# Performance work log

Measured on AMD Instinct MI355X. Metric: run time of the kernel, lower is better.

Reference implementation:

```python
import jax, jax.numpy as jnp
import numpy as np

B, N, D, H, L = 128, 256, 256, 8, 4      # graphs, nodes/graph, hidden, heads, layers
NTOT = B * N                              # 32768 nodes
E = 1048576                               # edges (avg degree 32)
DIN = 64
DH = D // H
BN_EPS = 1e-5
BN_SCALE = 1.0 / np.sqrt(1.0 + BN_EPS)    # eval BN with running mean 0, var 1


def _bn(h, g, b):
    # eval-mode BatchNorm1d: (h - 0)/sqrt(1 + eps) * g + b
    return h * (g * BN_SCALE) + b


def setup_inputs() -> dict:
    key = jax.random.key(0)
    ks = jax.random.split(key, 32)
    s = 0.02
    x = jax.random.normal(ks[0], (NTOT, DIN), jnp.float32)
    # within-graph random edges: dst lives in the same graph as src
    src = jax.random.randint(ks[1], (E,), 0, NTOT, dtype=jnp.int32)
    dst = (src // N) * N + jax.random.randint(ks[2], (E,), 0, N, dtype=jnp.int32)
    edge_index = jnp.stack([src, dst])
    edge_attr = jax.random.uniform(ks[3], (E,), jnp.float32)
    batch = jnp.arange(NTOT, dtype=jnp.int32) // N
    inp = {
        "x": x,
        "edge_attr": edge_attr,
        "node_w": s * jax.random.normal(ks[4], (DIN, D), jnp.float32),
        "node_b": jnp.zeros((D,), jnp.float32),
        "edge_w": s * jax.random.normal(ks[5], (1, D), jnp.float32),
        "edge_b": jnp.zeros((D,), jnp.float32),
        "gine_w1": s * jax.random.normal(ks[6], (L, D, D), jnp.float32),
        "gine_b1": jnp.zeros((L, D), jnp.float32),
        "gine_w2": s * jax.random.normal(ks[7], (L, D, D), jnp.float32),
        "gine_b2": jnp.zeros((L, D), jnp.float32),
        "attn_in_w": s * jax.random.normal(ks[8], (L, D, 3 * D), jnp.float32),
        "attn_in_b": jnp.zeros((L, 3 * D), jnp.float32),
        "attn_out_w": s * jax.random.normal(ks[9], (L, D, D), jnp.float32),
        "attn_out_b": jnp.zeros((L, D), jnp.float32),
        "mlp_w1": s * jax.random.normal(ks[10], (L, D, 2 * D), jnp.float32),
        "mlp_b1": jnp.zeros((L, 2 * D), jnp.float32),
        "mlp_w2": s * jax.random.normal(ks[11], (L, 2 * D, D), jnp.float32),
        "mlp_b2": jnp.zeros((L, D), jnp.float32),
        "bn1_g": 1.0 + 0.1 * jax.random.normal(ks[12], (L, D), jnp.float32),
        "bn1_b": jnp.zeros((L, D), jnp.float32),
        "bn2_g": 1.0 + 0.1 * jax.random.normal(ks[13], (L, D), jnp.float32),
        "bn2_b": jnp.zeros((L, D), jnp.float32),
        "bn3_g": 1.0 + 0.1 * jax.random.normal(ks[14], (L, D), jnp.float32),
        "bn3_b": jnp.zeros((L, D), jnp.float32),
        "edge_index": edge_index,
        "batch": batch,
    }
    return inp


def reference(x, edge_attr, node_w, node_b, edge_w, edge_b,
              gine_w1, gine_b1, gine_w2, gine_b2,
              attn_in_w, attn_in_b, attn_out_w, attn_out_b,
              mlp_w1, mlp_b1, mlp_w2, mlp_b2,
              bn1_g, bn1_b, bn2_g, bn2_b, bn3_g, bn3_b,
              edge_index, batch):
    src, dst = edge_index[0], edge_index[1]
    h = x @ node_w + node_b                                  # [NTOT, D]
    e = edge_attr[:, None] * edge_w[0] + edge_b              # [E, D] (Linear(1, D))
    scale = 1.0 / np.sqrt(DH)
    for l in range(L):
        # --- GINEConv: out = mlp((1+eps)*x + sum_j relu(x_j + e_ij)), eps=0 ---
        msg = jax.nn.relu(h[src] + e)                        # [E, D] gather
        agg = jax.ops.segment_sum(msg, dst, num_segments=NTOT)  # scatter-add
        z = h + agg
        z = jax.nn.relu(z @ gine_w1[l] + gine_b1[l]) @ gine_w2[l] + gine_b2[l]
        h1 = _bn(z + h, bn1_g[l], bn1_b[l])                  # local branch + residual
        # --- global multi-head self-attention per graph (dense batch, no padding) ---
        hd = h.reshape(B, N, D)
        qkv = hd @ attn_in_w[l] + attn_in_b[l]               # [B, N, 3D]
        q, k, v = jnp.split(qkv, 3, axis=-1)
        q = q.reshape(B, N, H, DH).transpose(0, 2, 1, 3)     # [B, H, N, DH]
        k = k.reshape(B, N, H, DH).transpose(0, 2, 1, 3)
        v = v.reshape(B, N, H, DH).transpose(0, 2, 1, 3)
        attn = jax.nn.softmax(jnp.einsum('bhqd,bhkd->bhqk', q, k) * scale, axis=-1)
        o = jnp.einsum('bhqk,bhkd->bhqd', attn, v).transpose(0, 2, 1, 3).reshape(B, N, D)
        o = (o @ attn_out_w[l] + attn_out_b[l]).reshape(NTOT, D)
        h2 = _bn(o + h, bn2_g[l], bn2_b[l])                  # global branch + residual
        # --- combine + FFN ---
        out = h1 + h2
        out = out + (jax.nn.relu(out @ mlp_w1[l] + mlp_b1[l]) @ mlp_w2[l] + mlp_b2[l])
        h = _bn(out, bn3_g[l], bn3_b[l])
    return h
```

## Files before the change

### kernel.cpp

```cpp
#include <hip/hip_runtime.h>
#include <math.h>

#define NTOT   32768
#define DMODEL 256
#define EDGES  1048576
#define BGRAPH 128
#define NNODE  256
#define NHEAD  8
#define DHEAD  32
#define NLAYER 4
#define DIN    64
#define BNS    0.9999950000374997f
#define CAPG   9216

typedef short bf16x8 __attribute__((ext_vector_type(8)));
typedef float f32x4  __attribute__((ext_vector_type(4)));

__device__ __forceinline__ unsigned short f2b(float f) {
    union { float f; unsigned int u; } v; v.f = f;
    unsigned int r = v.u + 0x7FFFu + ((v.u >> 16) & 1u);
    return (unsigned short)(r >> 16);
}
__device__ __forceinline__ float b2f(unsigned short u) {
    union { unsigned int u; float f; } v; v.u = ((unsigned int)u) << 16;
    return v.f;
}

__global__ __launch_bounds__(1024)
void k_bucket(const int* __restrict__ src, const int* __restrict__ dst,
              const float* __restrict__ ea, int* __restrict__ gcnt,
              uint2* __restrict__ gbuf) {
    __shared__ int hist[BGRAPH], base[BGRAPH], cur[BGRAPH];
    int t = threadIdx.x;
    int e0 = blockIdx.x * 4096;
    if (t < BGRAPH) { hist[t] = 0; cur[t] = 0; }
    __syncthreads();
    int g4[4]; unsigned int m4[4], a4[4];
#pragma unroll
    for (int j = 0; j < 4; ++j) {
        int e = e0 + j * 1024 + t;
        int s = src[e], d = dst[e];
        g4[j] = d >> 8;
        m4[j] = (unsigned int)(s & 255) | ((unsigned int)(d & 255) << 16);
        a4[j] = __float_as_uint(ea[e]);
        atomicAdd(&hist[g4[j]], 1);
    }
    __syncthreads();
    if (t < BGRAPH) base[t] = atomicAdd(&gcnt[t], hist[t]);
    __syncthreads();
#pragma unroll
    for (int j = 0; j < 4; ++j) {
        int g = g4[j];
        int slot = base[g] + atomicAdd(&cur[g], 1);
        if (slot < CAPG) {
            uint2 r; r.x = m4[j]; r.y = a4[j];
            gbuf[(size_t)g * CAPG + slot] = r;
        }
    }
}

__global__ __launch_bounds__(1024)
void k_gsort(const uint2* __restrict__ gbuf, const int* __restrict__ gcnt,
             uint2* __restrict__ epk, int* __restrict__ rowptr) {
    __shared__ int s[NNODE], excl[NNODE + 1], cur[NNODE];
    int g = blockIdx.x;
    int c = gcnt[g];
    int t = threadIdx.x;
    size_t base = (size_t)g * CAPG;
    if (t < NNODE) { s[t] = 0; cur[t] = 0; }
    __syncthreads();
    for (int i = t; i < c; i += 1024)
        atomicAdd(&s[gbuf[base + i].x >> 16], 1);
    __syncthreads();
    for (int o = 1; o < NNODE; o <<= 1) {
        int add = (t < NNODE && t >= o) ? s[t - o] : 0;
        __syncthreads();
        if (t < NNODE) s[t] += add;
        __syncthreads();
    }
    if (t < NNODE) excl[t + 1] = s[t];
    if (t == 0) excl[0] = 0;
    __syncthreads();
    if (t <= NNODE) rowptr[g * (NNODE + 1) + t] = (int)base + excl[t];
    for (int i = t; i < c; i += 1024) {
        uint2 r = gbuf[base + i];
        int dl = r.x >> 16;
        int p = excl[dl] + atomicAdd(&cur[dl], 1);
        epk[base + p] = r;
    }
}

__global__ __launch_bounds__(256)
void k_convall(const float* __restrict__ node_w, const float* __restrict__ gine_w1,
               const float* __restrict__ gine_w2, const float* __restrict__ attn_out_w,
               const float* __restrict__ attn_in_w, const float* __restrict__ mlp_w1,
               const float* __restrict__ mlp_w2,
               const float* __restrict__ bn1_g, const float* __restrict__ bn1_b,
               const float* __restrict__ bn2_g, const float* __restrict__ bn2_b,
               const float* __restrict__ bn3_g, const float* __restrict__ bn3_b,
               const float* __restrict__ gb2, const float* __restrict__ aob,
               const float* __restrict__ mb2, const float* __restrict__ x,
               unsigned short* __restrict__ w_node, unsigned short* __restrict__ w_g1,
               unsigned short* __restrict__ w_cat, unsigned short* __restrict__ w_ai,
               unsigned short* __restrict__ w_m1, unsigned short* __restrict__ w_m2s,
               float* __restrict__ biasC, float* __restrict__ rC,
               float* __restrict__ biasF, float* __restrict__ rF,
               unsigned short* __restrict__ xb) {
    __shared__ float tile[32][33];
    int bid = blockIdx.x;
    int t = threadIdx.x;

    if (bid >= 2580) {
        int i = ((bid - 2580) * 256 + t) * 4;
        float4 v = *(const float4*)(x + i);
        xb[i + 0] = f2b(v.x); xb[i + 1] = f2b(v.y);
        xb[i + 2] = f2b(v.z); xb[i + 3] = f2b(v.w);
        return;
    }
    if (bid >= 2576) {
        int i = (bid - 2576) * 256 + t;
        float s1 = bn1_g[i] * BNS, t1 = bn1_b[i];
        float s2 = bn2_g[i] * BNS, t2 = bn2_b[i];
        float s3 = bn3_g[i] * BNS, t3 = bn3_b[i];
        biasC[i] = gb2[i] * s1 + t1 + aob[i] * s2 + t2;
        rC[i]    = s1 + s2;
        biasF[i] = mb2[i] * s3 + t3;
        rF[i]    = s3;
        return;
    }
    const float* src; unsigned short* dst; const float* scale;
    int K_, N_, Kdst, koff, tx, ty, local;
    if (bid < 16)        { local = bid;      src = node_w;     dst = w_node; scale = nullptr; K_ = 64;  N_ = 256; Kdst = 64;  koff = 0;   tx = 8;  ty = 2;  }
    else if (bid < 272)  { local = bid-16;   src = gine_w1;    dst = w_g1;   scale = nullptr; K_ = 256; N_ = 256; Kdst = 256; koff = 0;   tx = 8;  ty = 8;  }
    else if (bid < 528)  { local = bid-272;  src = gine_w2;    dst = w_cat;  scale = bn1_g;   K_ = 256; N_ = 256; Kdst = 512; koff = 0;   tx = 8;  ty = 8;  }
    else if (bid < 784)  { local = bid-528;  src = attn_out_w; dst = w_cat;  scale = bn2_g;   K_ = 256; N_ = 256; Kdst = 512; koff = 256; tx = 8;  ty = 8;  }
    else if (bid < 1552) { local = bid-784;  src = attn_in_w;  dst = w_ai;   scale = nullptr; K_ = 256; N_ = 768; Kdst = 256; koff = 0;   tx = 24; ty = 8;  }
    else if (bid < 2064) { local = bid-1552; src = mlp_w1;     dst = w_m1;   scale = nullptr; K_ = 256; N_ = 512; Kdst = 256; koff = 0;   tx = 16; ty = 8;  }
    else                 { local = bid-2064; src = mlp_w2;     dst = w_m2s;  scale = bn3_g;   K_ = 512; N_ = 256; Kdst = 512; koff = 0;   tx = 8;  ty = 16; }
    int per = tx * ty;
    int l = local / per;
    int rem = local - l * per;
    int kyt = rem / tx, nxt = rem - kyt * tx;
    int n0 = nxt * 32, k0 = kyt * 32;
    const float* s = src + (size_t)l * K_ * N_;
    unsigned short* d = dst + (size_t)l * N_ * Kdst;
    int tx2 = t & 31, ty2 = t >> 5;
#pragma unroll
    for (int i = 0; i < 32; i += 8)
        tile[ty2 + i][tx2] = s[(size_t)(k0 + ty2 + i) * N_ + n0 + tx2];
    __syncthreads();
#pragma unroll
    for (int i = 0; i < 32; i += 8) {
        int n = n0 + ty2 + i;
        float sc = scale ? scale[(size_t)l * N_ + n] * BNS : 1.f;
        d[(size_t)n * Kdst + koff + k0 + tx2] = f2b(tile[tx2][ty2 + i] * sc);
    }
}

__global__ __launch_bounds__(1024)
void k_gine_g1(const unsigned short* __restrict__ hb,
               const int* __restrict__ rowptr, const uint2* __restrict__ epk,
               const float* __restrict__ ew, const float* __restrict__ eb,
               const unsigned short* __restrict__ w1,
               const float* __restrict__ b1,
               unsigned short* __restrict__ hid) {
    __shared__ unsigned short lds_h[NNODE * DMODEL];
    __shared__ uint2 mscr[16][64];
    int g = blockIdx.x >> 1, half = blockIdx.x & 1;
    int t = threadIdx.x;

    const unsigned short* gsrc = hb + (size_t)g * NNODE * DMODEL;
#pragma unroll
    for (int i = 0; i < 8; ++i) {
        int slot = i * 1024 + t;
        __builtin_amdgcn_global_load_lds(
            (const __attribute__((address_space(1))) void*)(gsrc + slot * 8),
            (__attribute__((address_space(3))) void*)&lds_h[slot * 8], 16, 0, 0);
    }
    asm volatile("s_waitcnt vmcnt(0)" ::: "memory");
    __syncthreads();

    int w = t >> 6, lane = t & 63;
    int d0 = lane * 4;
    float4 ew4 = *(const float4*)&ew[d0];
    float4 eb4 = *(const float4*)&eb[d0];
    uint2* ms = mscr[w];

    const int* rp = rowptr + g * (NNODE + 1);
    int ln0 = half * 128 + w * 8;
    unsigned int zlo[8], zhi[8];
#pragma unroll 1
    for (int i = 0; i < 8; ++i) {
        int ln = ln0 + i;
        int beg = rp[ln], end = rp[ln + 1];
        float a0 = 0.f, a1 = 0.f, a2 = 0.f, a3 = 0.f;
        for (int c = beg; c < end; c += 64) {
            int cnt = min(64, end - c);
            if (lane < cnt) ms[lane] = epk[c + lane];
            asm volatile("s_waitcnt lgkmcnt(0)" ::: "memory");
#pragma unroll 4
            for (int ii = 0; ii < cnt; ++ii) {
                uint2 rec = ms[ii];
                int   sl  = (int)(rec.x & 0xffffu);
                float av  = __uint_as_float(rec.y);
                uint2 hv = *(const uint2*)&lds_h[sl * DMODEL + d0];
                float t0 = fmaf(av, ew4.x, eb4.x);
                float t1 = fmaf(av, ew4.y, eb4.y);
                float t2 = fmaf(av, ew4.z, eb4.z);
                float t3 = fmaf(av, ew4.w, eb4.w);
                a0 += fmaxf(__uint_as_float(hv.x << 16) + t0, 0.f);
                a1 += fmaxf(__uint_as_float(hv.x & 0xffff0000u) + t1, 0.f);
                a2 += fmaxf(__uint_as_float(hv.y << 16) + t2, 0.f);
                a3 += fmaxf(__uint_as_float(hv.y & 0xffff0000u) + t3, 0.f);
            }
        }
        uint2 hv = *(const uint2*)&lds_h[ln * DMODEL + d0];
        float z0 = __uint_as_float(hv.x << 16)         + a0;
        float z1 = __uint_as_float(hv.x & 0xffff0000u) + a1;
        float z2 = __uint_as_float(hv.y << 16)         + a2;
        float z3 = __uint_as_float(hv.y & 0xffff0000u) + a3;
        asm("v_cvt_pk_bf16_f32 %0, %1, %2" : "=v"(zlo[i]) : "v"(z0), "v"(z1));
        asm("v_cvt_pk_bf16_f32 %0, %1, %2" : "=v"(zhi[i]) : "v"(z2), "v"(z3));
    }
    __syncthreads();

    char* zs = (char*)lds_h;
#pragma unroll
    for (int i = 0; i < 8; ++i) {
        int r = w * 8 + i;
        int pq = (lane >> 1) ^ (r & 7);
        uint2 pk; pk.x = zlo[i]; pk.y = zhi[i];
        *(uint2*)(zs + r * 512 + (pq << 4) + ((lane & 1) << 3)) = pk;
    }
    __syncthreads();

    int wr2 = w >> 3, wc2 = w & 7;
    int rl = lane & 15, kc = lane >> 4;
    f32x4 acc[4][2] = {};
#pragma unroll
    for (int kq = 0; kq < 8; ++kq) {
        bf16x8 av[4], bv[2];
#pragma unroll
        for (int mm = 0; mm < 4; ++mm) {
            int r = wr2 * 64 + mm * 16 + rl;
            int pq = (kq * 4 + kc) ^ (r & 7);
            av[mm] = *(const bf16x8*)(zs + r * 512 + (pq << 4));
        }
#pragma unroll
        for (int nn = 0; nn < 2; ++nn) {
            int nrow = wc2 * 32 + nn * 16 + rl;
            bv[nn] = *(const bf16x8*)(w1 + (size_t)nrow * 256 + kq * 32 + kc * 8);
        }
        __builtin_amdgcn_s_setprio(1);
#pragma unroll
        for (int mm = 0; mm < 4; ++mm)
#pragma unroll
            for (int nn = 0; nn < 2; ++nn)
                acc[mm][nn] = __builtin_amdgcn_mfma_f32_16x16x32_bf16(av[mm], bv[nn], acc[mm][nn], 0, 0, 0);
        __builtin_amdgcn_s_setprio(0);
    }
    int rh = lane >> 4;
    size_t rowbase = (size_t)g * NNODE + half * 128;
#pragma unroll
    for (int nn = 0; nn < 2; ++nn) {
        int col = wc2 * 32 + nn * 16 + rl;
        float bb = b1[col];
#pragma unroll
        for (int mm = 0; mm < 4; ++mm) {
#pragma unroll
            for (int j = 0; j < 4; ++j) {
                int r = wr2 * 64 + mm * 16 + rh * 4 + j;
                float v = fmaxf(acc[mm][nn][j] + bb, 0.f);
                hid[(rowbase + r) * 512 + col] = f2b(v);
            }
        }
    }
}

template <int MODE>
__global__ __launch_bounds__(256)
void k_mm(const unsigned short* __restrict__ A, const unsigned short* __restrict__ Bt,
          const float* __restrict__ bias, float* __restrict__ Cf,
          unsigned short* __restrict__ Cb, int M, int N, int K, int ldc, int gx) {
    const int BM = 128, BN = 128, BK = 64;
    __shared__ unsigned short As[BM * BK];
    __shared__ unsigned short Bs[BN * BK];

    int nwg = gridDim.x;
    int bid = blockIdx.x;
    int logical = (bid & 7) * (nwg >> 3) + (bid >> 3);
    int by = logical / gx, bx = logical % gx;

    int t = threadIdx.x;
    int w = t >> 6, l = t & 63;
    int wr = w >> 1, wc = w & 1;
    int bm = by * BM, bn = bx * BN;

    f32x4 acc[4][4] = {};
    int rl = l & 15, kc = l >> 4;

    for (int k0 = 0; k0 < K; k0 += BK) {
#pragma unroll
        for (int i = 0; i < 4; ++i) {
            int slot = i * 256 + t;
            int row = slot >> 3, pc = slot & 7;
            int lc = pc ^ (row & 7);
            const unsigned short* gp = A + (size_t)(bm + row) * K + k0 + lc * 8;
            __builtin_amdgcn_global_load_lds(
                (const __attribute__((address_space(1))) void*)gp,
                (__attribute__((address_space(3))) void*)&As[(i * 256 + w * 64) * 8],
                16, 0, 0);
        }
#pragma unroll
        for (int i = 0; i < 4; ++i) {
            int slot = i * 256 + t;
            int row = slot >> 3, pc = slot & 7;
            int lc = pc ^ (row & 7);
            const unsigned short* gp = Bt + (size_t)(bn + row) * K + k0 + lc * 8;
            __builtin_amdgcn_global_load_lds(
                (const __attribute__((address_space(1))) void*)gp,
                (__attribute__((address_space(3))) void*)&Bs[(i * 256 + w * 64) * 8],
                16, 0, 0);
        }
        asm volatile("s_waitcnt vmcnt(0)" ::: "memory");
        __syncthreads();

#pragma unroll
        for (int kk = 0; kk < 2; ++kk) {
            int lch = kk * 4 + kc;
            bf16x8 av[4], bv[4];
#pragma unroll
            for (int m = 0; m < 4; ++m) {
                int r = wr * 64 + m * 16 + rl;
                av[m] = *(const bf16x8*)&As[r * BK + ((lch ^ (r & 7)) << 3)];
            }
#pragma unroll
            for (int n = 0; n < 4; ++n) {
                int r = wc * 64 + n * 16 + rl;
                bv[n] = *(const bf16x8*)&Bs[r * BK + ((lch ^ (r & 7)) << 3)];
            }
#pragma unroll
            for (int m = 0; m < 4; ++m)
#pragma unroll
                for (int n = 0; n < 4; ++n)
                    acc[m][n] = __builtin_amdgcn_mfma_f32_16x16x32_bf16(av[m], bv[n], acc[m][n], 0, 0, 0);
        }
        __syncthreads();
    }

    int rh = l >> 4;
#pragma unroll
    for (int n = 0; n < 4; ++n) {
        int col = bn + wc * 64 + n * 16 + rl;
        float bv_ = bias[col];
#pragma unroll
        for (int m = 0; m < 4; ++m) {
#pragma unroll
            for (int j = 0; j < 4; ++j) {
                int row = bm + wr * 64 + m * 16 + rh * 4 + j;
                size_t idx = (size_t)row * ldc + col;
                float v = acc[m][n][j] + bv_;
                if (MODE == 1) v = fmaxf(v, 0.f);
                if (Cf) Cf[idx] = v;
                Cb[idx] = f2b(v);
            }
        }
    }
}

#define VP 264
#define OSTR 512
#define OOFF 256
__global__ __launch_bounds__(256, 3)
void k_attn(const unsigned short* __restrict__ qkv, unsigned short* __restrict__ o) {
    __shared__ unsigned short lds[8448 + 16896];
    unsigned short* Vt = lds;
    unsigned short* Ps = lds + 8448;

    int bh = blockIdx.x;
    int b = bh >> 3, h = bh & 7;
    int t = threadIdx.x;
    int w = t >> 6, l = t & 63;
    int rl = l & 15, kc = l >> 4;
    const float scale = 0.17677669529663687f;

    const unsigned short* base = qkv + (size_t)b * NNODE * (3 * DMODEL);
    const unsigned short* Kbase = base + DMODEL + h * DHEAD;

    {
        int k0 = (t & 63) * 4, d0 = (t >> 6) * 8;
        bf16x8 vr[4];
#pragma unroll
        for (int i = 0; i < 4; ++i)
            vr[i] = *(const bf16x8*)(base + (size_t)(k0 + i) * (3 * DMODEL) + 2 * DMODEL + h * DHEAD + d0);
#pragma unroll
        for (int d = 0; d < 8; ++d) {
            ushort4 pk;
            pk.x = (unsigned short)vr[0][d];
            pk.y = (unsigned short)vr[1][d];
            pk.z = (unsigned short)vr[2][d];
            pk.w = (unsigned short)vr[3][d];
            *(ushort4*)&Vt[(d0 + d) * VP + k0] = pk;
        }
    }

    bf16x8 qv[4];
#pragma unroll
    for (int m = 0; m < 4; ++m) {
        int q = w * 64 + m * 16 + rl;
        qv[m] = *(const bf16x8*)(base + (size_t)q * (3 * DMODEL) + h * DHEAD + kc * 8);
    }
    __syncthreads();

    unsigned short* Pw = Ps + w * 16 * VP;
    f32x4 zero = {0.f, 0.f, 0.f, 0.f};

#pragma unroll 1
    for (int m = 0; m < 4; ++m) {
        f32x4 s[16];
#pragma unroll
        for (int g4 = 0; g4 < 4; ++g4) {
            bf16x8 kv[4];
#pragma unroll
            for (int i = 0; i < 4; ++i)
                kv[i] = *(const bf16x8*)(Kbase + (size_t)((g4 * 4 + i) * 16 + rl) * (3 * DMODEL) + kc * 8);
            __builtin_amdgcn_s_setprio(1);
#pragma unroll
            for (int i = 0; i < 4; ++i)
                s[g4 * 4 + i] = __builtin_amdgcn_mfma_f32_16x16x32_bf16(kv[i], qv[m], zero, 0, 0, 0);
            __builtin_amdgcn_s_setprio(0);
        }
        float mv = -1e30f;
#pragma unroll
        for (int n = 0; n < 16; ++n)
#pragma unroll
            for (int j = 0; j < 4; ++j) mv = fmaxf(mv, s[n][j]);
        mv = fmaxf(mv, __shfl_xor(mv, 16));
        mv = fmaxf(mv, __shfl_xor(mv, 32));
        float nb = -mv * scale;
        float sumv = 0.f;
#pragma unroll
        for (int n = 0; n < 16; ++n) {
            float p0 = __expf(fmaf(s[n][0], scale, nb));
            float p1 = __expf(fmaf(s[n][1], scale, nb));
            float p2 = __expf(fmaf(s[n][2], scale, nb));
            float p3 = __expf(fmaf(s[n][3], scale, nb));
            sumv += (p0 + p1) + (p2 + p3);
            unsigned int lo, hi;
            asm("v_cvt_pk_bf16_f32 %0, %1, %2" : "=v"(lo) : "v"(p0), "v"(p1));
            asm("v_cvt_pk_bf16_f32 %0, %1, %2" : "=v"(hi) : "v"(p2), "v"(p3));
            uint2 pk; pk.x = lo; pk.y = hi;
            *(uint2*)&Pw[rl * VP + n * 16 + kc * 4] = pk;
        }
        sumv += __shfl_xor(sumv, 16);
        sumv += __shfl_xor(sumv, 32);

        f32x4 o0 = zero, o1 = zero;
#pragma unroll
        for (int ks = 0; ks < 8; ++ks) {
            bf16x8 pa = *(const bf16x8*)&Pw[rl * VP + ks * 32 + kc * 8];
            bf16x8 v0 = *(const bf16x8*)&Vt[rl * VP + ks * 32 + kc * 8];
            bf16x8 v1 = *(const bf16x8*)&Vt[(16 + rl) * VP + ks * 32 + kc * 8];
            __builtin_amdgcn_s_setprio(1);
            o0 = __builtin_amdgcn_mfma_f32_16x16x32_bf16(pa, v0, o0, 0, 0, 0);
            o1 = __builtin_amdgcn_mfma_f32_16x16x32_bf16(pa, v1, o1, 0, 0, 0);
            __builtin_amdgcn_s_setprio(0);
        }
#pragma unroll
        for (int j = 0; j < 4; ++j) {
            float sj = __shfl(sumv, kc * 4 + j);
            float inv = 1.f / sj;
            int q = w * 64 + m * 16 + kc * 4 + j;
            unsigned short* orow = o + ((size_t)b * NNODE + q) * OSTR + OOFF + h * DHEAD;
            orow[rl]      = f2b(o0[j] * inv);
            orow[16 + rl] = f2b(o1[j] * inv);
        }
    }
}

template <int LAST>
__global__ __launch_bounds__(512)
void k_tail(const unsigned short* __restrict__ comb2,
            const unsigned short* __restrict__ hbin,
            const unsigned short* __restrict__ wc,
            const unsigned short* __restrict__ m1,
            const unsigned short* __restrict__ m2s,
            const float* __restrict__ biasC, const float* __restrict__ rC,
            const float* __restrict__ b1,
            const float* __restrict__ biasF, const float* __restrict__ rF,
            unsigned short* __restrict__ hbout, float* __restrict__ outf) {
    __shared__ unsigned short WS[8192];
    __shared__ unsigned short cmbS[32768];
    __shared__ unsigned short hidS[32768];
    unsigned short* AS = hidS;

    int bm = blockIdx.x * 128;
    int t = threadIdx.x;
    int w = t >> 6, l = t & 63;
    int rl = l & 15, kc = l >> 4;
    int node = w * 16 + rl;
    size_t gnode = (size_t)(bm + node);
    char* cS = (char*)cmbS;
    char* hS = (char*)hidS;

    int row0 = t >> 2, q0 = t & 3;
    int slot1 = 512 + t, row1 = slot1 >> 2, q1 = slot1 & 3;
    int lq0 = (q0 - (row0 >> 1)) & 3;
    int lq1 = (q1 - (row1 >> 1)) & 3;

    f32x4 accC[16] = {};

    {
        const unsigned short* wp0 = wc + (size_t)row0 * 512 + lq0 * 8;
        const unsigned short* wp1 = wc + (size_t)row1 * 512 + lq1 * 8;
        const unsigned short* ap0 = comb2 + (size_t)(bm + row0) * 512 + lq0 * 8;
        uint4 rw0 = *(const uint4*)(wp0);
        uint4 rw1 = *(const uint4*)(wp1);
        uint4 ra0 = *(const uint4*)(ap0);
        *(uint4*)&WS[t * 8]     = rw0;
        *(uint4*)&WS[slot1 * 8] = rw1;
        *(uint4*)&AS[t * 8]     = ra0;
        __syncthreads();

        f32x4 accA[16] = {};
        for (int ks = 0; ks < 16; ++ks) {
            if (ks < 15) {
                rw0 = *(const uint4*)(wp0 + (ks + 1) * 32);
                rw1 = *(const uint4*)(wp1 + (ks + 1) * 32);
                ra0 = *(const uint4*)(ap0 + (ks + 1) * 32);
            }
            bf16x8 b = *(const bf16x8*)&AS[node * 32 + (((kc + (node >> 1)) & 3) << 3)];
            __builtin_amdgcn_s_setprio(1);
#pragma unroll
            for (int mf = 0; mf < 16; ++mf) {
                int row = mf * 16 + rl;
                bf16x8 a = *(const bf16x8*)&WS[row * 32 + (((kc + (row >> 1)) & 3) << 3)];
                accA[mf] = __builtin_amdgcn_mfma_f32_16x16x32_bf16(a, b, accA[mf], 0, 0, 0);
            }
            __builtin_amdgcn_s_setprio(0);
            __syncthreads();
            if (ks < 15) {
                *(uint4*)&WS[t * 8]     = rw0;
                *(uint4*)&WS[slot1 * 8] = rw1;
                *(uint4*)&AS[t * 8]     = ra0;
            }
            __syncthreads();
        }
#pragma unroll
        for (int mf = 0; mf < 16; ++mf) {
            int dim0 = mf * 16 + kc * 4;
            float4 bc = *(const float4*)&biasC[dim0];
            float4 rc = *(const float4*)&rC[dim0];
            uint2 hv = *(const uint2*)&hbin[gnode * 256 + dim0];
            float v0 = accA[mf][0] + bc.x + rc.x * __uint_as_float(hv.x << 16);
            float v1 = accA[mf][1] + bc.y + rc.y * __uint_as_float(hv.x & 0xffff0000u);
            float v2 = accA[mf][2] + bc.z + rc.z * __uint_as_float(hv.y << 16);
            float v3 = accA[mf][3] + bc.w + rc.w * __uint_as_float(hv.y & 0xffff0000u);
            unsigned int lo, hi;
            asm("v_cvt_pk_bf16_f32 %0, %1, %2" : "=v"(lo) : "v"(v0), "v"(v1));
            asm("v_cvt_pk_bf16_f32 %0, %1, %2" : "=v"(hi) : "v"(v2), "v"(v3));
            uint2 pk; pk.x = lo; pk.y = hi;
            int q = dim0 >> 3, half = (dim0 >> 2) & 1;
            *(uint2*)(cS + node * 512 + ((q ^ (node & 7)) << 4) + (half << 3)) = pk;
        }
    }
    __syncthreads();

    for (int nh = 0; nh < 2; ++nh) {
        {
            const unsigned short* bp0 = m1 + (size_t)(nh * 256 + row0) * 256 + lq0 * 8;
            const unsigned short* bp1 = m1 + (size_t)(nh * 256 + row1) * 256 + lq1 * 8;
            uint4 rw0 = *(const uint4*)(bp0);
            uint4 rw1 = *(const uint4*)(bp1);
            *(uint4*)&WS[t * 8]     = rw0;
            *(uint4*)&WS[slot1 * 8] = rw1;
            __syncthreads();

            f32x4 accB[16] = {};
            for (int ks = 0; ks < 8; ++ks) {
                if (ks < 7) {
                    rw0 = *(const uint4*)(bp0 + (ks + 1) * 32);
                    rw1 = *(const uint4*)(bp1 + (ks + 1) * 32);
                }
                int kq = ks * 4 + kc;
                bf16x8 b = *(const bf16x8*)(cS + node * 512 + ((kq ^ (node & 7)) << 4));
                __builtin_amdgcn_s_setprio(1);
#pragma unroll
                for (int mf = 0; mf < 16; ++mf) {
                    int row = mf * 16 + rl;
                    bf16x8 a = *(const bf16x8*)&WS[row * 32 + (((kc + (row >> 1)) & 3) << 3)];
                    accB[mf] = __builtin_amdgcn_mfma_f32_16x16x32_bf16(a, b, accB[mf], 0, 0, 0);
                }
                __builtin_amdgcn_s_setprio(0);
                __syncthreads();
                if (ks < 7) {
                    *(uint4*)&WS[t * 8]     = rw0;
                    *(uint4*)&WS[slot1 * 8] = rw1;
                }
                __syncthreads();
            }
#pragma unroll
            for (int mf = 0; mf < 16; ++mf) {
                int dim0 = mf * 16 + kc * 4;
                float4 bb = *(const float4*)&b1[nh * 256 + dim0];
                float v0 = fmaxf(accB[mf][0] + bb.x, 0.f);
                float v1 = fmaxf(accB[mf][1] + bb.y, 0.f);
                float v2 = fmaxf(accB[mf][2] + bb.z, 0.f);
                float v3 = fmaxf(accB[mf][3] + bb.w, 0.f);
                unsigned int lo, hi;
                asm("v_cvt_pk_bf16_f32 %0, %1, %2" : "=v"(lo) : "v"(v0), "v"(v1));
                asm("v_cvt_pk_bf16_f32 %0, %1, %2" : "=v"(hi) : "v"(v2), "v"(v3));
                uint2 pk; pk.x = lo; pk.y = hi;
                int q = dim0 >> 3, half = (dim0 >> 2) & 1;
                *(uint2*)(hS + node * 512 + ((q ^ (node & 7)) << 4) + (half << 3)) = pk;
            }
        }
        __syncthreads();
        {
            const unsigned short* cp0 = m2s + (size_t)row0 * 512 + nh * 256 + lq0 * 8;
            const unsigned short* cp1 = m2s + (size_t)row1 * 512 + nh * 256 + lq1 * 8;
            uint4 rw0 = *(const uint4*)(cp0);
            uint4 rw1 = *(const uint4*)(cp1);
            *(uint4*)&WS[t * 8]     = rw0;
            *(uint4*)&WS[slot1 * 8] = rw1;
            __syncthreads();

            for (int ks = 0; ks < 8; ++ks) {
                if (ks < 7) {
                    rw0 = *(const uint4*)(cp0 + (ks + 1) * 32);
                    rw1 = *(const uint4*)(cp1 + (ks + 1) * 32);
                }
                int kq = ks * 4 + kc;
                bf16x8 b = *(const bf16x8*)(hS + node * 512 + ((kq ^ (node & 7)) << 4));
                __builtin_amdgcn_s_setprio(1);
#pragma unroll
                for (int mf = 0; mf < 16; ++mf) {
                    int row = mf * 16 + rl;
                    bf16x8 a = *(const bf16x8*)&WS[row * 32 + (((kc + (row >> 1)) & 3) << 3)];
                    accC[mf] = __builtin_amdgcn_mfma_f32_16x16x32_bf16(a, b, accC[mf], 0, 0, 0);
                }
                __builtin_amdgcn_s_setprio(0);
                __syncthreads();
                if (ks < 7) {
                    *(uint4*)&WS[t * 8]     = rw0;
                    *(uint4*)&WS[slot1 * 8] = rw1;
                }
                __syncthreads();
            }
        }
    }

    if (LAST) {
#pragma unroll
        for (int mf = 0; mf < 16; ++mf) {
            int dim0 = mf * 16 + kc * 4;
            float4 bf_ = *(const float4*)&biasF[dim0];
            float4 rf = *(const float4*)&rF[dim0];
            int q = dim0 >> 3, half = (dim0 >> 2) & 1;
            uint2 cv = *(const uint2*)(cS + node * 512 + ((q ^ (node & 7)) << 4) + (half << 3));
            float4 o4;
            o4.x = accC[mf][0] + bf_.x + rf.x * __uint_as_float(cv.x << 16);
            o4.y = accC[mf][1] + bf_.y + rf.y * __uint_as_float(cv.x & 0xffff0000u);
            o4.z = accC[mf][2] + bf_.z + rf.z * __uint_as_float(cv.y << 16);
            o4.w = accC[mf][3] + bf_.w + rf.w * __uint_as_float(cv.y & 0xffff0000u);
            *(float4*)&outf[gnode * 256 + dim0] = o4;
        }
    } else {
        __syncthreads();
#pragma unroll
        for (int mf = 0; mf < 16; ++mf) {
            int dim0 = mf * 16 + kc * 4;
            float4 bf_ = *(const float4*)&biasF[dim0];
            float4 rf = *(const float4*)&rF[dim0];
            int q = dim0 >> 3, half = (dim0 >> 2) & 1;
            uint2 cv = *(const uint2*)(cS + node * 512 + ((q ^ (node & 7)) << 4) + (half << 3));
            float v0 = accC[mf][0] + bf_.x + rf.x * __uint_as_float(cv.x << 16);
            float v1 = accC[mf][1] + bf_.y + rf.y * __uint_as_float(cv.x & 0xffff0000u);
            float v2 = accC[mf][2] + bf_.z + rf.z * __uint_as_float(cv.y << 16);
            float v3 = accC[mf][3] + bf_.w + rf.w * __uint_as_float(cv.y & 0xffff0000u);
            unsigned int lo, hi;
            asm("v_cvt_pk_bf16_f32 %0, %1, %2" : "=v"(lo) : "v"(v0), "v"(v1));
            asm("v_cvt_pk_bf16_f32 %0, %1, %2" : "=v"(hi) : "v"(v2), "v"(v3));
            uint2 pk; pk.x = lo; pk.y = hi;
            *(uint2*)(hS + node * 512 + ((q ^ (node & 7)) << 4) + (half << 3)) = pk;
        }
        __syncthreads();
#pragma unroll
        for (int it = 0; it < 8; ++it) {
            int slot = it * 512 + t;
            int n = slot >> 5, p = slot & 31;
            uint4 v4 = *(const uint4*)(hS + n * 512 + p * 16);
            int lq = p ^ (n & 7);
            *(uint4*)&hbout[(size_t)(bm + n) * 256 + lq * 8] = v4;
        }
    }
}

extern "C" void kernel_launch(void* const* d_in, const int* in_sizes, int n_in,
                              void* d_out, int out_size, void* d_ws, size_t ws_size,
                              hipStream_t stream) {
    const float* x          = (const float*)d_in[0];
    const float* edge_attr  = (const float*)d_in[1];
    const float* node_w     = (const float*)d_in[2];
    const float* node_b     = (const float*)d_in[3];
    const float* edge_w     = (const float*)d_in[4];
    const float* edge_b     = (const float*)d_in[5];
    const float* gine_w1    = (const float*)d_in[6];
    const float* gine_b1    = (const float*)d_in[7];
    const float* gine_w2    = (const float*)d_in[8];
    const float* gine_b2    = (const float*)d_in[9];
    const float* attn_in_w  = (const float*)d_in[10];
    const float* attn_in_b  = (const float*)d_in[11];
    const float* attn_out_w = (const float*)d_in[12];
    const float* attn_out_b = (const float*)d_in[13];
    const float* mlp_w1     = (const float*)d_in[14];
    const float* mlp_b1     = (const float*)d_in[15];
    const float* mlp_w2     = (const float*)d_in[16];
    const float* mlp_b2     = (const float*)d_in[17];
    const float* bn1_g      = (const float*)d_in[18];
    const float* bn1_b      = (const float*)d_in[19];
    const float* bn2_g      = (const float*)d_in[20];
    const float* bn2_b      = (const float*)d_in[21];
    const float* bn3_g      = (const float*)d_in[22];
    const float* bn3_b      = (const float*)d_in[23];
    const int*   edge_index = (const int*)d_in[24];

    const int* srcp = edge_index;
    const int* dstp = edge_index + EDGES;

    float* out = (float*)d_out;
    char*  ws  = (char*)d_ws;

    size_t off = 0;
    unsigned short* hb    = (unsigned short*)(ws + off); off += (size_t)NTOT * DMODEL * 2;
    unsigned short* comb2 = (unsigned short*)(ws + off); off += (size_t)NTOT * 512 * 2;
    unsigned short* qkvb  = (unsigned short*)(ws + off); off += (size_t)NTOT * 768 * 2;
    unsigned short* xb    = (unsigned short*)(ws + off); off += (size_t)NTOT * DIN * 2;
    unsigned short* w_node = (unsigned short*)(ws + off); off += (size_t)DMODEL * DIN * 2;
    unsigned short* w_g1   = (unsigned short*)(ws + off); off += (size_t)NLAYER * DMODEL * DMODEL * 2;
    unsigned short* w_cat  = (unsigned short*)(ws + off); off += (size_t)NLAYER * DMODEL * 512 * 2;
    unsigned short* w_ai   = (unsigned short*)(ws + off); off += (size_t)NLAYER * 3 * DMODEL * DMODEL * 2;
    unsigned short* w_m1   = (unsigned short*)(ws + off); off += (size_t)NLAYER * 2 * DMODEL * DMODEL * 2;
    unsigned short* w_m2s  = (unsigned short*)(ws + off); off += (size_t)NLAYER * DMODEL * 512 * 2;
    float* biasC = (float*)(ws + off); off += (size_t)NLAYER * DMODEL * 4;
    float* rC    = (float*)(ws + off); off += (size_t)NLAYER * DMODEL * 4;
    float* biasF = (float*)(ws + off); off += (size_t)NLAYER * DMODEL * 4;
    float* rF    = (float*)(ws + off); off += (size_t)NLAYER * DMODEL * 4;
    uint2* gbuf  = (uint2*)(ws + off);  off += (size_t)BGRAPH * CAPG * 8;
    uint2* epk   = (uint2*)(ws + off);  off += (size_t)BGRAPH * CAPG * 8;
    int*   gcnt  = (int*)(ws + off);    off += (size_t)BGRAPH * 4;
    int*   rowptr = (int*)(ws + off);   off += (size_t)BGRAPH * (NNODE + 1) * 4;
    (void)ws_size; (void)in_sizes; (void)n_in; (void)out_size;

    hipMemsetAsync(gcnt, 0, (size_t)BGRAPH * 4, stream);
    k_bucket<<<EDGES / 4096, 1024, 0, stream>>>(srcp, dstp, edge_attr, gcnt, gbuf);
    k_gsort<<<BGRAPH, 1024, 0, stream>>>(gbuf, gcnt, epk, rowptr);

    k_convall<<<4628, 256, 0, stream>>>(node_w, gine_w1, gine_w2, attn_out_w,
                                        attn_in_w, mlp_w1, mlp_w2,
                                        bn1_g, bn1_b, bn2_g, bn2_b, bn3_g, bn3_b,
                                        gine_b2, attn_out_b, mlp_b2, x,
                                        w_node, w_g1, w_cat, w_ai, w_m1, w_m2s,
                                        biasC, rC, biasF, rF, xb);

    k_mm<0><<<2 * (NTOT / 128), 256, 0, stream>>>(
        xb, w_node, node_b, nullptr, hb, NTOT, DMODEL, DIN, DMODEL, 2);

    for (int l = 0; l < NLAYER; ++l) {
        const unsigned short* g1 = w_g1 + (size_t)l * DMODEL * DMODEL;
        const unsigned short* wc = w_cat + (size_t)l * DMODEL * 512;
        const unsigned short* ai = w_ai + (size_t)l * 3 * DMODEL * DMODEL;
        const unsigned short* m1 = w_m1 + (size_t)l * 2 * DMODEL * DMODEL;
        const unsigned short* m2 = w_m2s + (size_t)l * DMODEL * 512;

        k_gine_g1<<<BGRAPH * 2, 1024, 0, stream>>>(hb, rowptr, epk, edge_w, edge_b,
                                                   g1, gine_b1 + (size_t)l * DMODEL, comb2);
        k_mm<0><<<6 * (NTOT / 128), 256, 0, stream>>>(
            hb, ai, attn_in_b + (size_t)l * 3 * DMODEL, nullptr,
            qkvb, NTOT, 3 * DMODEL, DMODEL, 3 * DMODEL, 6);
        k_attn<<<BGRAPH * NHEAD, 256, 0, stream>>>(qkvb, comb2);
        if (l == NLAYER - 1)
            k_tail<1><<<NTOT / 128, 512, 0, stream>>>(
                comb2, hb, wc, m1, m2,
                biasC + (size_t)l * DMODEL, rC + (size_t)l * DMODEL,
                mlp_b1 + (size_t)l * 2 * DMODEL,
                biasF + (size_t)l * DMODEL, rF + (size_t)l * DMODEL,
                hb, out);
        else
            k_tail<0><<<NTOT / 128, 512, 0, stream>>>(
                comb2, hb, wc, m1, m2,
                biasC + (size_t)l * DMODEL, rC + (size_t)l * DMODEL,
                mlp_b1 + (size_t)l * 2 * DMODEL,
                biasF + (size_t)l * DMODEL, rF + (size_t)l * DMODEL,
                hb, nullptr);
    }
}
```

Before: 716.1 us.

## Gather GINE neighbor features from global memory instead of staging graph in LDS

```diff
diff --git a/kernel.cpp b/kernel.cpp
--- a/kernel.cpp
+++ b/kernel.cpp
@@ -157,34 +157,26 @@
     }
 }
 
-__global__ __launch_bounds__(1024)
+__global__ __launch_bounds__(1024, 8)
 void k_gine_g1(const unsigned short* __restrict__ hb,
                const int* __restrict__ rowptr, const uint2* __restrict__ epk,
                const float* __restrict__ ew, const float* __restrict__ eb,
                const unsigned short* __restrict__ w1,
                const float* __restrict__ b1,
                unsigned short* __restrict__ hid) {
-    __shared__ unsigned short lds_h[NNODE * DMODEL];
+    __shared__ unsigned short zs16[128 * 256];
     __shared__ uint2 mscr[16][64];
-    int g = blockIdx.x >> 1, half = blockIdx.x & 1;
+    int bid = blockIdx.x;
+    int logical = (bid & 7) * (BGRAPH * 2 / 8) + (bid >> 3);
+    int g = logical >> 1, half = logical & 1;
     int t = threadIdx.x;
-
-    const unsigned short* gsrc = hb + (size_t)g * NNODE * DMODEL;
-#pragma unroll
-    for (int i = 0; i < 8; ++i) {
-        int slot = i * 1024 + t;
-        __builtin_amdgcn_global_load_lds(
-            (const __attribute__((address_space(1))) void*)(gsrc + slot * 8),
-            (__attribute__((address_space(3))) void*)&lds_h[slot * 8], 16, 0, 0);
-    }
-    asm volatile("s_waitcnt vmcnt(0)" ::: "memory");
-    __syncthreads();
 
     int w = t >> 6, lane = t & 63;
     int d0 = lane * 4;
     float4 ew4 = *(const float4*)&ew[d0];
     float4 eb4 = *(const float4*)&eb[d0];
     uint2* ms = mscr[w];
+    const unsigned short* hg = hb + (size_t)g * NNODE * DMODEL;
 
     const int* rp = rowptr + g * (NNODE + 1);
     int ln0 = half * 128 + w * 8;
@@ -203,7 +195,8 @@
                 uint2 rec = ms[ii];
                 int   sl  = (int)(rec.x & 0xffffu);
                 float av  = __uint_as_float(rec.y);
-                uint2 hv = *(const uint2*)&lds_h[sl * DMODEL + d0];
+                int   hoff = sl * DMODEL + d0;
+                uint2 hv = *(const uint2*)&hg[hoff];
                 float t0 = fmaf(av, ew4.x, eb4.x);
                 float t1 = fmaf(av, ew4.y, eb4.y);
                 float t2 = fmaf(av, ew4.z, eb4.z);
@@ -214,17 +207,16 @@
                 a3 += fmaxf(__uint_as_float(hv.y & 0xffff0000u) + t3, 0.f);
             }
         }
-        uint2 hv = *(const uint2*)&lds_h[ln * DMODEL + d0];
-        float z0 = __uint_as_float(hv.x << 16)         + a0;
-        float z1 = __uint_as_float(hv.x & 0xffff0000u) + a1;
-        float z2 = __uint_as_float(hv.y << 16)         + a2;
-        float z3 = __uint_as_float(hv.y & 0xffff0000u) + a3;
+        uint2 hv2 = *(const uint2*)&hg[ln * DMODEL + d0];
+        float z0 = __uint_as_float(hv2.x << 16)         + a0;
+        float z1 = __uint_as_float(hv2.x & 0xffff0000u) + a1;
+        float z2 = __uint_as_float(hv2.y << 16)         + a2;
+        float z3 = __uint_as_float(hv2.y & 0xffff0000u) + a3;
         asm("v_cvt_pk_bf16_f32 %0, %1, %2" : "=v"(zlo[i]) : "v"(z0), "v"(z1));
         asm("v_cvt_pk_bf16_f32 %0, %1, %2" : "=v"(zhi[i]) : "v"(z2), "v"(z3));
     }
-    __syncthreads();
-
-    char* zs = (char*)lds_h;
+
+    char* zs = (char*)zs16;
 #pragma unroll
     for (int i = 0; i < 8; ++i) {
         int r = w * 8 + i;
```

Result: slower. 835.5 us (+16.7%).
